# Kernel optimization log

Hardware: AMD Instinct MI355X
Metric: run time of the kernel (lower is better)

## Reference

```python
import math
import jax, jax.numpy as jnp
import numpy as np

EPS = 1e-6
MAX_SCALE_LOG = math.log(100.0)

def rms_norm(x, scale, eps=EPS):
    # x * scale / rms(x), reduction over last dim
    ms = jnp.mean(jnp.square(x), axis=-1, keepdims=True)
    return x * (scale * jax.lax.rsqrt(ms + eps))

def axial_rope_theta(pos, n_heads, d_head, dtype):
    # freqs: linspace in log-space from pi to 10*pi, reshaped to [n_heads, d_head//4]
    f = np.exp(np.linspace(math.log(math.pi), math.log(10.0 * math.pi),
                           n_heads * d_head // 4 + 1)[:-1])
    freqs = jnp.asarray(f.reshape(d_head // 4, n_heads).T, dtype)  # [h, e/4]
    theta_h = pos[:, :, None, 0:1] * freqs  # [n, l, h, e/4]
    theta_w = pos[:, :, None, 1:2] * freqs  # [n, l, h, e/4]
    theta = jnp.concatenate([theta_h, theta_w], axis=-1)  # [n, l, h, e/2]
    return theta.transpose(0, 2, 1, 3)  # [n, h, l, e/2]

def apply_rotary(x, theta):
    d = theta.shape[-1]
    x1, x2, x3 = x[..., :d], x[..., d:2 * d], x[..., 2 * d:]
    cos, sin = jnp.cos(theta), jnp.sin(theta)
    return jnp.concatenate([x1 * cos - x2 * sin, x2 * cos + x1 * sin, x3], axis=-1)

def setup_inputs() -> dict:
    key = jax.random.key(0)
    ks = jax.random.split(key, 8)
    n, l, d_model, d_head = 2, 2048, 1024, 64
    n_heads = d_model // d_head
    x = jax.random.normal(ks[0], (n, l, d_model), jnp.float32)
    pos = jax.random.uniform(ks[1], (n, l, 2), jnp.float32)
    cond = jax.random.normal(ks[2], (n, 1, d_model), jnp.float32)
    # params (torch uses zero-init for w_cond/w_out; small random for a non-degenerate baseline)
    w_cond = jax.random.normal(ks[3], (d_model, d_model), jnp.float32) * 0.02
    w_qkv = jax.random.normal(ks[4], (d_model, 3 * d_model), jnp.float32) * (d_model ** -0.5)
    qk_scale = jnp.full((n_heads,), math.log(10.0), jnp.float32)
    w_out = jax.random.normal(ks[5], (d_model, d_model), jnp.float32) * 0.02
    return {"x": x, "pos": pos, "cond": cond, "w_cond": w_cond,
            "w_qkv": w_qkv, "qk_scale": qk_scale, "w_out": w_out}

def reference(x, pos, cond, w_cond, w_qkv, qk_scale, w_out):
    n, l, d_model = x.shape
    h = qk_scale.shape[0]
    e = d_model // h
    # AdaRMSNorm: scale = linear(cond) + 1
    xn = rms_norm(x, cond @ w_cond + 1.0)
    # QKV projection
    q, k, v = jnp.split(xn @ w_qkv, 3, axis=-1)
    to_heads = lambda t: t.reshape(n, l, h, e).transpose(0, 2, 1, 3)  # [n,h,l,e]
    q, k, v = to_heads(q), to_heads(k), to_heads(v)
    # QKNorm: per-head learned scale, rms over head dim
    s = jnp.exp(0.5 * jnp.minimum(qk_scale, MAX_SCALE_LOG) - 0.25 * math.log(e))
    q = rms_norm(q, s[:, None, None])
    k = rms_norm(k, s[:, None, None])
    # Axial RoPE
    theta = axial_rope_theta(pos, h, e, x.dtype)
    q = apply_rotary(q, theta)
    k = apply_rotary(k, theta)
    # SDPA (no mask)
    attn = jax.nn.softmax(jnp.einsum('nhqe,nhke->nhqk', q, k) / math.sqrt(e), axis=-1)
    o = jnp.einsum('nhqk,nhke->nhqe', attn, v)
    o = o.transpose(0, 2, 1, 3).reshape(n, l, d_model)
    return o @ w_out
```

## Files before the change

kernel.cpp:

```cpp
#include <hip/hip_runtime.h>

typedef unsigned short u16;
typedef unsigned int u32;
typedef short s16x8 __attribute__((ext_vector_type(8)));
typedef short s16x4 __attribute__((ext_vector_type(4)));
typedef float f32x4 __attribute__((ext_vector_type(4)));
typedef u32 u32x2 __attribute__((ext_vector_type(2)));

#define AS1 __attribute__((address_space(1)))
#define AS3 __attribute__((address_space(3)))

__device__ __forceinline__ float bf2f(u16 u) {
    union { unsigned int i; float f; } x; x.i = ((unsigned int)u) << 16; return x.f;
}
__device__ __forceinline__ u16 f2bf(float f) {
    union { float f; unsigned int i; } x; x.f = f;
    unsigned int r = (x.i + 0x7FFFu + ((x.i >> 16) & 1u)) >> 16;
    return (u16)r;
}
__device__ __forceinline__ void storeOut(u16* p, float v) { *p = f2bf(v); }
__device__ __forceinline__ void storeOut(float* p, float v) { *p = v; }
__device__ __forceinline__ float loadIn(const void* p, size_t i, int isf32) {
    return isf32 ? ((const float*)p)[i] : bf2f(((const u16*)p)[i]);
}
__device__ __forceinline__ float fexp2(float x) {
#if __has_builtin(__builtin_amdgcn_exp2f)
    return __builtin_amdgcn_exp2f(x);
#else
    return exp2f(x);
#endif
}
__device__ __forceinline__ u32 pack_bf(float a, float b) {
    u32 ua = __float_as_uint(a) + 0x8000u;
    u32 ub = __float_as_uint(b) + 0x8000u;
    return __builtin_amdgcn_perm(ub, ua, 0x07060302u);
}

__global__ __launch_bounds__(256) void detect_dtype(const u16* __restrict__ x,
                                                    int* __restrict__ flag) {
    __shared__ int cnt[4];
    const int tid = threadIdx.x;
    int c = 0;
    #pragma unroll
    for (int i = 0; i < 4; ++i) {
        const u16 u = x[tid * 4 + i];
        const int e = (u >> 7) & 0xFF;
        c += (e >= 101 && e <= 135) ? 1 : 0;
    }
    #pragma unroll
    for (int m = 1; m < 64; m <<= 1) c += __shfl_xor(c, m, 64);
    if ((tid & 63) == 0) cnt[tid >> 6] = c;
    __syncthreads();
    if (tid == 0) {
        const int t = cnt[0] + cnt[1] + cnt[2] + cnt[3];
        *flag = (t < 800) ? 1 : 0;
    }
}

__global__ __launch_bounds__(256) void cond_gemv(const void* __restrict__ cond,
                                                 const void* __restrict__ w,
                                                 float* __restrict__ out,
                                                 const int* __restrict__ flag) {
    const int isf32 = *flag;
    const int d  = blockIdx.x * 256 + threadIdx.x;
    const int n  = blockIdx.y;
    const int k0 = blockIdx.z * 64;
    float acc = 0.f;
    #pragma unroll 8
    for (int k = 0; k < 64; ++k)
        acc += loadIn(cond, n * 1024 + k0 + k, isf32) *
               loadIn(w, (size_t)(k0 + k) * 1024 + d, isf32);
    atomicAdd(out + n * 1024 + d, acc);
}

__global__ __launch_bounds__(256) void rmsnorm_x(const void* __restrict__ x,
                                                 const float* __restrict__ scl,
                                                 u16* __restrict__ xn,
                                                 const int* __restrict__ flag) {
    const int isf32 = *flag;
    const int tok = blockIdx.x;
    const int n = tok >> 11;
    u16* orow = xn + (size_t)tok * 1024;
    const int base = threadIdx.x * 4;
    float f0, f1, f2, f3;
    if (isf32) {
        const float4 v = *(const float4*)((const float*)x + (size_t)tok * 1024 + base);
        f0 = v.x; f1 = v.y; f2 = v.z; f3 = v.w;
    } else {
        s16x4 uv = *(const s16x4*)((const u16*)x + (size_t)tok * 1024 + base);
        f0 = bf2f((u16)uv[0]); f1 = bf2f((u16)uv[1]); f2 = bf2f((u16)uv[2]); f3 = bf2f((u16)uv[3]);
    }
    float ss = f0 * f0 + f1 * f1 + f2 * f2 + f3 * f3;
    #pragma unroll
    for (int m = 1; m < 64; m <<= 1) ss += __shfl_xor(ss, m, 64);
    __shared__ float red[4];
    const int wave = threadIdx.x >> 6, lane = threadIdx.x & 63;
    if (lane == 0) red[wave] = ss;
    __syncthreads();
    float ms = (red[0] + red[1] + red[2] + red[3]) * (1.f / 1024.f);
    float rinv = rsqrtf(ms + 1e-6f);
    orow[base + 0] = f2bf(f0 * (scl[n * 1024 + base + 0] + 1.f) * rinv);
    orow[base + 1] = f2bf(f1 * (scl[n * 1024 + base + 1] + 1.f) * rinv);
    orow[base + 2] = f2bf(f2 * (scl[n * 1024 + base + 2] + 1.f) * rinv);
    orow[base + 3] = f2bf(f3 * (scl[n * 1024 + base + 3] + 1.f) * rinv);
}

__global__ __launch_bounds__(256) void transpose_bf(const void* __restrict__ src,
                                                    u16* __restrict__ dst, int R, int C,
                                                    const int* __restrict__ flag) {
    const int isf32 = *flag;
    __shared__ u16 t[32][33];
    const int c0 = blockIdx.x * 32, r0 = blockIdx.y * 32;
    const int tx = threadIdx.x & 31, ty = threadIdx.x >> 5;
    #pragma unroll
    for (int i = 0; i < 4; ++i)
        t[ty + i * 8][tx] = f2bf(loadIn(src, (size_t)(r0 + ty + i * 8) * C + c0 + tx, isf32));
    __syncthreads();
    #pragma unroll
    for (int i = 0; i < 4; ++i)
        dst[(size_t)(c0 + ty + i * 8) * R + r0 + tx] = t[tx][ty + i * 8];
}

__global__ __launch_bounds__(256) void transpose_v(const u16* __restrict__ qkv,
                                                   u16* __restrict__ vtg) {
    __shared__ u16 t[64][65];
    const int nh = blockIdx.y, l0 = blockIdx.x * 64;
    const int n = nh >> 4, h = nh & 15;
    const int tid = threadIdx.x;
    const u16* src = qkv + (size_t)(n * 2048 + l0) * 3072 + 2048 + h * 64;
    #pragma unroll
    for (int it = 0; it < 16; ++it) {
        const int idx = it * 256 + tid;
        const int row = idx >> 6, col = idx & 63;
        t[row][col] = src[(size_t)row * 3072 + col];
    }
    __syncthreads();
    u16* dst = vtg + (size_t)nh * 64 * 2048 + l0;
    #pragma unroll
    for (int it = 0; it < 16; ++it) {
        const int idx = it * 256 + tid;
        const int er = idx >> 6, lc = idx & 63;
        dst[(size_t)er * 2048 + lc] = t[lc][er];
    }
}

template <typename OutT>
__global__ __launch_bounds__(256) void gemm_bt(const u16* __restrict__ A,
                                               const u16* __restrict__ BT,
                                               OutT* __restrict__ C, int Nn, int K) {
    __shared__ u16 As[128 * 32];
    __shared__ u16 Bs[128 * 32];
    const int tid = threadIdx.x;
    const int wave = tid >> 6, lane = tid & 63;
    const int l15 = lane & 15, quad = lane >> 4;
    const int bm0 = blockIdx.y * 128, bn0 = blockIdx.x * 128;
    const int wr = wave >> 1, wc = wave & 1;
    f32x4 acc[4][4] = {};
    const int srow = lane >> 2;
    const int g = (lane & 3) ^ (srow & 3);
    for (int bk = 0; bk < K; bk += 32) {
        __syncthreads();
        #pragma unroll
        for (int p = 0; p < 2; ++p) {
            const int rowl = p * 64 + wave * 16 + srow;
            const u16* ga = A + (size_t)(bm0 + rowl) * K + bk + g * 8;
            u16* la = As + (p * 64 + wave * 16) * 32;
            __builtin_amdgcn_global_load_lds((const AS1 void*)ga, (AS3 void*)la, 16, 0, 0);
            const u16* gb = BT + (size_t)(bn0 + rowl) * K + bk + g * 8;
            u16* lb = Bs + (p * 64 + wave * 16) * 32;
            __builtin_amdgcn_global_load_lds((const AS1 void*)gb, (AS3 void*)lb, 16, 0, 0);
        }
        __syncthreads();
        s16x8 af[4], bfr[4];
        #pragma unroll
        for (int mt = 0; mt < 4; ++mt) {
            const int r = wr * 64 + mt * 16 + l15;
            af[mt] = *(const s16x8*)(As + r * 32 + ((quad ^ (r & 3)) << 3));
        }
        #pragma unroll
        for (int nt = 0; nt < 4; ++nt) {
            const int r = wc * 64 + nt * 16 + l15;
            bfr[nt] = *(const s16x8*)(Bs + r * 32 + ((quad ^ (r & 3)) << 3));
        }
        #pragma unroll
        for (int mt = 0; mt < 4; ++mt)
            #pragma unroll
            for (int nt = 0; nt < 4; ++nt)
                acc[mt][nt] = __builtin_amdgcn_mfma_f32_16x16x32_bf16(af[mt], bfr[nt], acc[mt][nt], 0, 0, 0);
    }
    #pragma unroll
    for (int mt = 0; mt < 4; ++mt)
        #pragma unroll
        for (int nt = 0; nt < 4; ++nt)
            #pragma unroll
            for (int r = 0; r < 4; ++r) {
                const int row = bm0 + wr * 64 + mt * 16 + quad * 4 + r;
                const int col = bn0 + wc * 64 + nt * 16 + l15;
                storeOut(C + (size_t)row * Nn + col, acc[mt][nt][r]);
            }
}

__global__ __launch_bounds__(256) void qk_head(const u16* __restrict__ qkv,
                                               const void* __restrict__ pos,
                                               const void* __restrict__ qk_scale,
                                               u16* __restrict__ q_ws,
                                               u16* __restrict__ k_ws,
                                               const int* __restrict__ flag) {
    const int isf32 = *flag;
    const int gw = blockIdx.x * 4 + (threadIdx.x >> 6);
    const int lane = threadIdx.x & 63;
    const int tok = gw >> 4, h = gw & 15;
    const int n = tok >> 11, l = tok & 2047;
    const u16* row = qkv + (size_t)tok * 3072;
    float qv = bf2f(row[h * 64 + lane]);
    float kv = bf2f(row[1024 + h * 64 + lane]);
    float q2 = qv * qv, k2 = kv * kv;
    #pragma unroll
    for (int m = 1; m < 64; m <<= 1) { q2 += __shfl_xor(q2, m, 64); k2 += __shfl_xor(k2, m, 64); }
    float qn = qv * rsqrtf(q2 * (1.f / 64.f) + 1e-6f);
    float kn = kv * rsqrtf(k2 * (1.f / 64.f) + 1e-6f);
    const float qs = loadIn(qk_scale, h, isf32);
    const float s = __expf(0.5f * fminf(qs, 4.605170186f) - 1.039720771f);
    qn *= s * s * 0.125f * 1.44269504089f;
    const int j = lane & 31;
    const float p = loadIn(pos, tok * 2 + (j >> 4), isf32);
    const float t = (float)((j & 15) * 16 + h);
    const float freq = 3.14159265358979f * __expf(t * (2.302585093f / 256.f));
    const float th = p * freq;
    const float c = __cosf(th), sn = __sinf(th);
    const float pq = __shfl_xor(qn, 32, 64);
    const float pk = __shfl_xor(kn, 32, 64);
    float qr, kr;
    if (lane < 32) { qr = qn * c - pq * sn; kr = kn * c - pk * sn; }
    else           { qr = qn * c + pq * sn; kr = kn * c + pk * sn; }
    const size_t oidx = ((size_t)(n * 16 + h) * 2048 + l) * 64 + lane;
    q_ws[oidx] = f2bf(qr);
    k_ws[oidx] = f2bf(kr);
}

__global__ __launch_bounds__(256, 2) void attn4(const u16* __restrict__ Q,
                                                const u16* __restrict__ K,
                                                const u16* __restrict__ Vtg,
                                                u16* __restrict__ O) {
    __shared__ u16 Ks[2][64 * 64];
    __shared__ u16 Vt[2][64 * 64];
    __shared__ u16 Ps[4][32 * 72];
    const int nh = blockIdx.y;
    const int q0 = blockIdx.x * 128;
    const int tid = threadIdx.x;
    const int wave = tid >> 6, lane = tid & 63;
    const int l15 = lane & 15, quad = lane >> 4;
    const size_t hb = (size_t)nh * 2048 * 64;
    const u16* Vbase = Vtg + (size_t)nh * 64 * 2048;

    const int dr0 = tid >> 3;
    const int dd  = tid & 7;

    s16x8 qf[2][2];
    #pragma unroll
    for (int qg = 0; qg < 2; ++qg)
        #pragma unroll
        for (int kc = 0; kc < 2; ++kc)
            qf[qg][kc] = *(const s16x8*)(Q + hb + (size_t)(q0 + wave * 32 + qg * 16 + l15) * 64 + kc * 32 + quad * 8);

    f32x4 Oacc[2][4] = {};
    float lacc[2] = {0.f, 0.f};
    u16* Pw = Ps[wave];

    #pragma unroll
    for (int it = 0; it < 2; ++it) {
        const int row = it * 32 + dr0;
        const int g = dd ^ (row & 7);
        __builtin_amdgcn_global_load_lds(
            (const AS1 void*)(K + hb + (size_t)row * 64 + g * 8),
            (AS3 void*)(Ks[0] + (it * 256 + wave * 64) * 8), 16, 0, 0);
        __builtin_amdgcn_global_load_lds(
            (const AS1 void*)(Vbase + (size_t)row * 2048 + g * 8),
            (AS3 void*)(Vt[0] + (it * 256 + wave * 64) * 8), 16, 0, 0);
    }
    __syncthreads();

    for (int i = 0; i < 32; ++i) {
        const int cur = i & 1;
        const int kb = i * 64;
        if (i < 31) {
            const int nxt = cur ^ 1;
            const int kbn = kb + 64;
            #pragma unroll
            for (int it = 0; it < 2; ++it) {
                const int row = it * 32 + dr0;
                const int g = dd ^ (row & 7);
                __builtin_amdgcn_global_load_lds(
                    (const AS1 void*)(K + hb + (size_t)(kbn + row) * 64 + g * 8),
                    (AS3 void*)(Ks[nxt] + (it * 256 + wave * 64) * 8), 16, 0, 0);
                __builtin_amdgcn_global_load_lds(
                    (const AS1 void*)(Vbase + (size_t)row * 2048 + kbn + g * 8),
                    (AS3 void*)(Vt[nxt] + (it * 256 + wave * 64) * 8), 16, 0, 0);
            }
        }

        f32x4 S[2][4] = {};
        #pragma unroll
        for (int kt = 0; kt < 4; ++kt) {
            const int r = kt * 16 + l15;
            #pragma unroll
            for (int kc = 0; kc < 2; ++kc) {
                const s16x8 kf = *(const s16x8*)(Ks[cur] + r * 64 + (((kc * 4 + quad) ^ (r & 7)) << 3));
                S[0][kt] = __builtin_amdgcn_mfma_f32_16x16x32_bf16(kf, qf[0][kc], S[0][kt], 0, 0, 0);
                S[1][kt] = __builtin_amdgcn_mfma_f32_16x16x32_bf16(kf, qf[1][kc], S[1][kt], 0, 0, 0);
            }
        }

        #pragma unroll
        for (int qg = 0; qg < 2; ++qg) {
            float rs = 0.f;
            #pragma unroll
            for (int kt = 0; kt < 4; ++kt) {
                const float e0 = fexp2(S[qg][kt][0] - 15.f);
                const float e1 = fexp2(S[qg][kt][1] - 15.f);
                const float e2 = fexp2(S[qg][kt][2] - 15.f);
                const float e3 = fexp2(S[qg][kt][3] - 15.f);
                rs += (e0 + e1) + (e2 + e3);
                u32x2 pk2;
                pk2[0] = pack_bf(e0, e1);
                pk2[1] = pack_bf(e2, e3);
                *(u32x2*)(Pw + (qg * 16 + l15) * 72 + kt * 16 + quad * 4) = pk2;
            }
            lacc[qg] += rs;
        }

        #pragma unroll
        for (int kc = 0; kc < 2; ++kc) {
            const s16x8 pf0 = *(const s16x8*)(Pw + l15 * 72 + kc * 32 + quad * 8);
            const s16x8 pf1 = *(const s16x8*)(Pw + (16 + l15) * 72 + kc * 32 + quad * 8);
            #pragma unroll
            for (int nto = 0; nto < 4; ++nto) {
                const int e = nto * 16 + l15;
                const s16x8 vf = *(const s16x8*)(Vt[cur] + e * 64 + (((kc * 4 + quad) ^ (e & 7)) << 3));
                Oacc[0][nto] = __builtin_amdgcn_mfma_f32_16x16x32_bf16(pf0, vf, Oacc[0][nto], 0, 0, 0);
                Oacc[1][nto] = __builtin_amdgcn_mfma_f32_16x16x32_bf16(pf1, vf, Oacc[1][nto], 0, 0, 0);
            }
        }

        if (i < 31) __syncthreads();
    }

    #pragma unroll
    for (int qg = 0; qg < 2; ++qg) {
        lacc[qg] += __shfl_xor(lacc[qg], 16, 64);
        lacc[qg] += __shfl_xor(lacc[qg], 32, 64);
    }

    const int n = nh >> 4, h = nh & 15;
    #pragma unroll
    for (int qg = 0; qg < 2; ++qg)
        #pragma unroll
        for (int r = 0; r < 4; ++r) {
            const float linv = 1.f / __shfl(lacc[qg], quad * 4 + r, 64);
            const int qrow = q0 + wave * 32 + qg * 16 + quad * 4 + r;
            #pragma unroll
            for (int nto = 0; nto < 4; ++nto)
                O[((size_t)n * 2048 + qrow) * 1024 + h * 64 + nto * 16 + l15] = f2bf(Oacc[qg][nto][r] * linv);
        }
}

extern "C" void kernel_launch(void* const* d_in, const int* in_sizes, int n_in,
                              void* d_out, int out_size, void* d_ws, size_t ws_size,
                              hipStream_t stream) {
    const void* x        = d_in[0];
    const void* pos      = d_in[1];
    const void* cond     = d_in[2];
    const void* w_cond   = d_in[3];
    const void* w_qkv    = d_in[4];
    const void* qk_scale = d_in[5];
    const void* w_out    = d_in[6];

    char* ws = (char*)d_ws;
    constexpr size_t OFS_SCALE = 0;
    constexpr size_t OFS_FLAG  = 8192;
    constexpr size_t OFS_XN    = 16384;
    constexpr size_t OFS_WQKVT = OFS_XN    + 8388608;
    constexpr size_t OFS_WOUTT = OFS_WQKVT + 6291456;
    constexpr size_t OFS_QKV   = OFS_WOUTT + 2097152;
    constexpr size_t OFS_Q     = OFS_QKV   + 25165824;
    constexpr size_t OFS_K     = OFS_Q     + 8388608;
    constexpr size_t OFS_VT    = OFS_K     + 8388608;
    constexpr size_t OFS_O     = OFS_VT    + 8388608;

    float* scale = (float*)(ws + OFS_SCALE);
    int*   flag  = (int*)(ws + OFS_FLAG);
    u16* xn    = (u16*)(ws + OFS_XN);
    u16* wqkvT = (u16*)(ws + OFS_WQKVT);
    u16* woutT = (u16*)(ws + OFS_WOUTT);
    u16* qkv   = (u16*)(ws + OFS_QKV);
    u16* qws   = (u16*)(ws + OFS_Q);
    u16* kws   = (u16*)(ws + OFS_K);
    u16* vtg   = (u16*)(ws + OFS_VT);
    u16* ows   = (u16*)(ws + OFS_O);

    detect_dtype<<<dim3(1), 256, 0, stream>>>((const u16*)x, flag);
    hipMemsetAsync(scale, 0, 2 * 1024 * sizeof(float), stream);
    cond_gemv<<<dim3(4, 2, 16), 256, 0, stream>>>(cond, w_cond, scale, flag);
    rmsnorm_x<<<dim3(4096), 256, 0, stream>>>(x, scale, xn, flag);
    transpose_bf<<<dim3(96, 32), 256, 0, stream>>>(w_qkv, wqkvT, 1024, 3072, flag);
    transpose_bf<<<dim3(32, 32), 256, 0, stream>>>(w_out, woutT, 1024, 1024, flag);
    gemm_bt<u16><<<dim3(24, 32), 256, 0, stream>>>(xn, wqkvT, qkv, 3072, 1024);
    qk_head<<<dim3(16384), 256, 0, stream>>>(qkv, pos, qk_scale, qws, kws, flag);
    transpose_v<<<dim3(32, 32), 256, 0, stream>>>(qkv, vtg);
    attn4<<<dim3(16, 32), 256, 0, stream>>>(qws, kws, vtg, ows);
    gemm_bt<float><<<dim3(8, 32), 256, 0, stream>>>(ows, woutT, (float*)d_out, 1024, 1024);
}
```

Baseline: 244.6 us.

## Fuse QK-norm/RoPE with V transpose and software-pipeline PV matmul in attention

```diff
diff --git a/kernel.cpp b/kernel.cpp
--- a/kernel.cpp
+++ b/kernel.cpp
@@ -121,29 +121,6 @@
         dst[(size_t)(c0 + ty + i * 8) * R + r0 + tx] = t[tx][ty + i * 8];
 }
 
-__global__ __launch_bounds__(256) void transpose_v(const u16* __restrict__ qkv,
-                                                   u16* __restrict__ vtg) {
-    __shared__ u16 t[64][65];
-    const int nh = blockIdx.y, l0 = blockIdx.x * 64;
-    const int n = nh >> 4, h = nh & 15;
-    const int tid = threadIdx.x;
-    const u16* src = qkv + (size_t)(n * 2048 + l0) * 3072 + 2048 + h * 64;
-    #pragma unroll
-    for (int it = 0; it < 16; ++it) {
-        const int idx = it * 256 + tid;
-        const int row = idx >> 6, col = idx & 63;
-        t[row][col] = src[(size_t)row * 3072 + col];
-    }
-    __syncthreads();
-    u16* dst = vtg + (size_t)nh * 64 * 2048 + l0;
-    #pragma unroll
-    for (int it = 0; it < 16; ++it) {
-        const int idx = it * 256 + tid;
-        const int er = idx >> 6, lc = idx & 63;
-        dst[(size_t)er * 2048 + lc] = t[lc][er];
-    }
-}
-
 template <typename OutT>
 __global__ __launch_bounds__(256) void gemm_bt(const u16* __restrict__ A,
                                                const u16* __restrict__ BT,
@@ -200,50 +177,77 @@
             }
 }
 
-__global__ __launch_bounds__(256) void qk_head(const u16* __restrict__ qkv,
-                                               const void* __restrict__ pos,
-                                               const void* __restrict__ qk_scale,
-                                               u16* __restrict__ q_ws,
-                                               u16* __restrict__ k_ws,
-                                               const int* __restrict__ flag) {
+__global__ __launch_bounds__(256) void qkv_head(const u16* __restrict__ qkv,
+                                                const void* __restrict__ pos,
+                                                const void* __restrict__ qk_scale,
+                                                u16* __restrict__ q_ws,
+                                                u16* __restrict__ k_ws,
+                                                u16* __restrict__ vtg,
+                                                const int* __restrict__ flag) {
     const int isf32 = *flag;
-    const int gw = blockIdx.x * 4 + (threadIdx.x >> 6);
-    const int lane = threadIdx.x & 63;
-    const int tok = gw >> 4, h = gw & 15;
-    const int n = tok >> 11, l = tok & 2047;
-    const u16* row = qkv + (size_t)tok * 3072;
-    float qv = bf2f(row[h * 64 + lane]);
-    float kv = bf2f(row[1024 + h * 64 + lane]);
-    float q2 = qv * qv, k2 = kv * kv;
-    #pragma unroll
-    for (int m = 1; m < 64; m <<= 1) { q2 += __shfl_xor(q2, m, 64); k2 += __shfl_xor(k2, m, 64); }
-    float qn = qv * rsqrtf(q2 * (1.f / 64.f) + 1e-6f);
-    float kn = kv * rsqrtf(k2 * (1.f / 64.f) + 1e-6f);
+    const int nh = blockIdx.y;
+    const int n = nh >> 4, h = nh & 15;
+    const int l0 = blockIdx.x * 64;
+    const int tid = threadIdx.x;
+    const int wave = tid >> 6, lane = tid & 63;
+
     const float qs = loadIn(qk_scale, h, isf32);
     const float s = __expf(0.5f * fminf(qs, 4.605170186f) - 1.039720771f);
-    qn *= s * s * 0.125f * 1.44269504089f;
+    const float qmul = s * s * 0.125f * 1.44269504089f;
     const int j = lane & 31;
-    const float p = loadIn(pos, tok * 2 + (j >> 4), isf32);
     const float t = (float)((j & 15) * 16 + h);
     const float freq = 3.14159265358979f * __expf(t * (2.302585093f / 256.f));
-    const float th = p * freq;
-    const float c = __cosf(th), sn = __sinf(th);
-    const float pq = __shfl_xor(qn, 32, 64);
-    const float pk = __shfl_xor(kn, 32, 64);
-    float qr, kr;
-    if (lane < 32) { qr = qn * c - pq * sn; kr = kn * c - pk * sn; }
-    else           { qr = qn * c + pq * sn; kr = kn * c + pk * sn; }
-    const size_t oidx = ((size_t)(n * 16 + h) * 2048 + l) * 64 + lane;
-    q_ws[oidx] = f2bf(qr);
-    k_ws[oidx] = f2bf(kr);
-}
-
-__global__ __launch_bounds__(256, 2) void attn4(const u16* __restrict__ Q,
+    const int pj = j >> 4;
+
+    #pragma unroll 2
+    for (int it = 0; it < 16; ++it) {
+        const int l = l0 + wave * 16 + it;
+        const int tok = n * 2048 + l;
+        const u16* row = qkv + (size_t)tok * 3072;
+        float qv = bf2f(row[h * 64 + lane]);
+        float kv = bf2f(row[1024 + h * 64 + lane]);
+        float q2 = qv * qv, k2 = kv * kv;
+        #pragma unroll
+        for (int m = 1; m < 64; m <<= 1) { q2 += __shfl_xor(q2, m, 64); k2 += __shfl_xor(k2, m, 64); }
+        float qn = qv * rsqrtf(q2 * (1.f / 64.f) + 1e-6f) * qmul;
+        float kn = kv * rsqrtf(k2 * (1.f / 64.f) + 1e-6f);
+        const float p = loadIn(pos, tok * 2 + pj, isf32);
+        const float th = p * freq;
+        const float c = __cosf(th), sn = __sinf(th);
+        const float pq = __shfl_xor(qn, 32, 64);
+        const float pk = __shfl_xor(kn, 32, 64);
+        float qr, kr;
+        if (lane < 32) { qr = qn * c - pq * sn; kr = kn * c - pk * sn; }
+        else           { qr = qn * c + pq * sn; kr = kn * c + pk * sn; }
+        const size_t oidx = ((size_t)nh * 2048 + l) * 64 + lane;
+        q_ws[oidx] = f2bf(qr);
+        k_ws[oidx] = f2bf(kr);
+    }
+
+    __shared__ u16 tbuf[64][65];
+    const u16* vsrc = qkv + (size_t)(n * 2048 + l0) * 3072 + 2048 + h * 64;
+    #pragma unroll
+    for (int it = 0; it < 16; ++it) {
+        const int idx = it * 256 + tid;
+        const int r = idx >> 6, c = idx & 63;
+        tbuf[r][c] = vsrc[(size_t)r * 3072 + c];
+    }
+    __syncthreads();
+    u16* dst = vtg + (size_t)nh * 131072 + l0;
+    #pragma unroll
+    for (int it = 0; it < 16; ++it) {
+        const int idx = it * 256 + tid;
+        const int er = idx >> 6, lc = idx & 63;
+        dst[(size_t)er * 2048 + lc] = tbuf[lc][er];
+    }
+}
+
+__global__ __launch_bounds__(256, 2) void attn5(const u16* __restrict__ Q,
                                                 const u16* __restrict__ K,
                                                 const u16* __restrict__ Vtg,
                                                 u16* __restrict__ O) {
     __shared__ u16 Ks[2][64 * 64];
-    __shared__ u16 Vt[2][64 * 64];
+    __shared__ u16 Vt[3][64 * 64];
     __shared__ u16 Ps[4][32 * 72];
     const int nh = blockIdx.y;
     const int q0 = blockIdx.x * 128;
@@ -251,8 +255,7 @@
     const int wave = tid >> 6, lane = tid & 63;
     const int l15 = lane & 15, quad = lane >> 4;
     const size_t hb = (size_t)nh * 2048 * 64;
-    const u16* Vbase = Vtg + (size_t)nh * 64 * 2048;
-
+    const u16* Vbase = Vtg + (size_t)nh * 131072;
     const int dr0 = tid >> 3;
     const int dd  = tid & 7;
 
@@ -280,46 +283,70 @@
     }
     __syncthreads();
 
+    int vprev = 2, vcur = 0, vnxt = 1;
+    s16x8 pf[2][2];
+
     for (int i = 0; i < 32; ++i) {
-        const int cur = i & 1;
-        const int kb = i * 64;
+        const int kcur = i & 1;
         if (i < 31) {
-            const int nxt = cur ^ 1;
-            const int kbn = kb + 64;
+            const int kbn = (i + 1) * 64;
             #pragma unroll
             for (int it = 0; it < 2; ++it) {
                 const int row = it * 32 + dr0;
                 const int g = dd ^ (row & 7);
                 __builtin_amdgcn_global_load_lds(
                     (const AS1 void*)(K + hb + (size_t)(kbn + row) * 64 + g * 8),
-                    (AS3 void*)(Ks[nxt] + (it * 256 + wave * 64) * 8), 16, 0, 0);
+                    (AS3 void*)(Ks[kcur ^ 1] + (it * 256 + wave * 64) * 8), 16, 0, 0);
                 __builtin_amdgcn_global_load_lds(
                     (const AS1 void*)(Vbase + (size_t)row * 2048 + kbn + g * 8),
-                    (AS3 void*)(Vt[nxt] + (it * 256 + wave * 64) * 8), 16, 0, 0);
-            }
-        }
-
-        f32x4 S[2][4] = {};
+                    (AS3 void*)(Vt[vnxt] + (it * 256 + wave * 64) * 8), 16, 0, 0);
+            }
+        }
+        if (i > 0) {
+            #pragma unroll
+            for (int kc = 0; kc < 2; ++kc) {
+                pf[kc][0] = *(const s16x8*)(Pw + l15 * 72 + kc * 32 + quad * 8);
+                pf[kc][1] = *(const s16x8*)(Pw + (16 + l15) * 72 + kc * 32 + quad * 8);
+            }
+        }
+        f32x4 S[2][4];
+        #pragma unroll
+        for (int qg = 0; qg < 2; ++qg)
+            #pragma unroll
+            for (int kt = 0; kt < 4; ++kt) {
+                S[qg][kt][0] = -15.f; S[qg][kt][1] = -15.f;
+                S[qg][kt][2] = -15.f; S[qg][kt][3] = -15.f;
+            }
         #pragma unroll
         for (int kt = 0; kt < 4; ++kt) {
             const int r = kt * 16 + l15;
             #pragma unroll
             for (int kc = 0; kc < 2; ++kc) {
-                const s16x8 kf = *(const s16x8*)(Ks[cur] + r * 64 + (((kc * 4 + quad) ^ (r & 7)) << 3));
+                const s16x8 kf = *(const s16x8*)(Ks[kcur] + r * 64 + (((kc * 4 + quad) ^ (r & 7)) << 3));
                 S[0][kt] = __builtin_amdgcn_mfma_f32_16x16x32_bf16(kf, qf[0][kc], S[0][kt], 0, 0, 0);
                 S[1][kt] = __builtin_amdgcn_mfma_f32_16x16x32_bf16(kf, qf[1][kc], S[1][kt], 0, 0, 0);
             }
         }
-
+        if (i > 0) {
+            #pragma unroll
+            for (int kc = 0; kc < 2; ++kc)
+                #pragma unroll
+                for (int nto = 0; nto < 4; ++nto) {
+                    const int e = nto * 16 + l15;
+                    const s16x8 vf = *(const s16x8*)(Vt[vprev] + e * 64 + (((kc * 4 + quad) ^ (e & 7)) << 3));
+                    Oacc[0][nto] = __builtin_amdgcn_mfma_f32_16x16x32_bf16(pf[kc][0], vf, Oacc[0][nto], 0, 0, 0);
+                    Oacc[1][nto] = __builtin_amdgcn_mfma_f32_16x16x32_bf16(pf[kc][1], vf, Oacc[1][nto], 0, 0, 0);
+                }
+        }
         #pragma unroll
         for (int qg = 0; qg < 2; ++qg) {
             float rs = 0.f;
             #pragma unroll
             for (int kt = 0; kt < 4; ++kt) {
-                const float e0 = fexp2(S[qg][kt][0] - 15.f);
-                const float e1 = fexp2(S[qg][kt][1] - 15.f);
-                const float e2 = fexp2(S[qg][kt][2] - 15.f);
-                const float e3 = fexp2(S[qg][kt][3] - 15.f);
+                const float e0 = fexp2(S[qg][kt][0]);
+                const float e1 = fexp2(S[qg][kt][1]);
+                const float e2 = fexp2(S[qg][kt][2]);
+                const float e3 = fexp2(S[qg][kt][3]);
                 rs += (e0 + e1) + (e2 + e3);
                 u32x2 pk2;
                 pk2[0] = pack_bf(e0, e1);
@@ -328,22 +355,24 @@
             }
             lacc[qg] += rs;
         }
-
-        #pragma unroll
-        for (int kc = 0; kc < 2; ++kc) {
-            const s16x8 pf0 = *(const s16x8*)(Pw + l15 * 72 + kc * 32 + quad * 8);
-            const s16x8 pf1 = *(const s16x8*)(Pw + (16 + l15) * 72 + kc * 32 + quad * 8);
-            #pragma unroll
-            for (int nto = 0; nto < 4; ++nto) {
-                const int e = nto * 16 + l15;
-                const s16x8 vf = *(const s16x8*)(Vt[cur] + e * 64 + (((kc * 4 + quad) ^ (e & 7)) << 3));
-                Oacc[0][nto] = __builtin_amdgcn_mfma_f32_16x16x32_bf16(pf0, vf, Oacc[0][nto], 0, 0, 0);
-                Oacc[1][nto] = __builtin_amdgcn_mfma_f32_16x16x32_bf16(pf1, vf, Oacc[1][nto], 0, 0, 0);
-            }
-        }
-
+        const int tmp = vprev; vprev = vcur; vcur = vnxt; vnxt = tmp;
         if (i < 31) __syncthreads();
     }
+
+    #pragma unroll
+    for (int kc = 0; kc < 2; ++kc) {
+        pf[kc][0] = *(const s16x8*)(Pw + l15 * 72 + kc * 32 + quad * 8);
+        pf[kc][1] = *(const s16x8*)(Pw + (16 + l15) * 72 + kc * 32 + quad * 8);
+    }
+    #pragma unroll
+    for (int kc = 0; kc < 2; ++kc)
+        #pragma unroll
+        for (int nto = 0; nto < 4; ++nto) {
+            const int e = nto * 16 + l15;
+            const s16x8 vf = *(const s16x8*)(Vt[vprev] + e * 64 + (((kc * 4 + quad) ^ (e & 7)) << 3));
+            Oacc[0][nto] = __builtin_amdgcn_mfma_f32_16x16x32_bf16(pf[kc][0], vf, Oacc[0][nto], 0, 0, 0);
+            Oacc[1][nto] = __builtin_amdgcn_mfma_f32_16x16x32_bf16(pf[kc][1], vf, Oacc[1][nto], 0, 0, 0);
+        }
 
     #pragma unroll
     for (int qg = 0; qg < 2; ++qg) {
@@ -405,8 +434,7 @@
     transpose_bf<<<dim3(96, 32), 256, 0, stream>>>(w_qkv, wqkvT, 1024, 3072, flag);
     transpose_bf<<<dim3(32, 32), 256, 0, stream>>>(w_out, woutT, 1024, 1024, flag);
     gemm_bt<u16><<<dim3(24, 32), 256, 0, stream>>>(xn, wqkvT, qkv, 3072, 1024);
-    qk_head<<<dim3(16384), 256, 0, stream>>>(qkv, pos, qk_scale, qws, kws, flag);
-    transpose_v<<<dim3(32, 32), 256, 0, stream>>>(qkv, vtg);
-    attn4<<<dim3(16, 32), 256, 0, stream>>>(qws, kws, vtg, ows);
+    qkv_head<<<dim3(32, 32), 256, 0, stream>>>(qkv, pos, qk_scale, qws, kws, vtg, flag);
+    attn5<<<dim3(16, 32), 256, 0, stream>>>(qws, kws, vtg, ows);
     gemm_bt<float><<<dim3(8, 32), 256, 0, stream>>>(ows, woutT, (float*)d_out, 1024, 1024);
 }
```

Measured after the change: 239.5 us. 1.02x faster.
